# Optimization experiments

Measured on AMD Instinct MI355X. Metric: run time of the kernel, lower is better.

The kernel has to match this reference:

```python
import jax, jax.numpy as jnp
import numpy as np

N = 100000
E = 1600000
IN_FEATS = 512
H1, F1 = 8, 8          # layer1: 8 heads x 8 units
H2, F2 = 1, 40         # layer2: 1 head x out_feats
NEG_SLOPE = 0.2


def setup_inputs() -> dict:
    key = jax.random.key(0)
    ks = jax.random.split(key, 12)
    x = jax.random.normal(ks[0], (N, IN_FEATS), dtype=jnp.float32)
    src = jax.random.randint(ks[1], (E,), 0, N, dtype=jnp.int32)
    dst = jax.random.randint(ks[2], (E,), 0, N, dtype=jnp.int32)
    # Xavier-ish init for params
    W1 = jax.random.normal(ks[3], (IN_FEATS, H1 * F1), dtype=jnp.float32) * (1.0 / np.sqrt(IN_FEATS))
    al1 = jax.random.normal(ks[4], (H1, F1), dtype=jnp.float32) * 0.1
    ar1 = jax.random.normal(ks[5], (H1, F1), dtype=jnp.float32) * 0.1
    b1 = jnp.zeros((H1 * F1,), dtype=jnp.float32)
    W2 = jax.random.normal(ks[6], (H1 * F1, H2 * F2), dtype=jnp.float32) * (1.0 / np.sqrt(H1 * F1))
    al2 = jax.random.normal(ks[7], (H2, F2), dtype=jnp.float32) * 0.1
    ar2 = jax.random.normal(ks[8], (H2, F2), dtype=jnp.float32) * 0.1
    b2 = jnp.zeros((H2 * F2,), dtype=jnp.float32)
    return {"x": x, "src": src, "dst": dst,
            "W1": W1, "al1": al1, "ar1": ar1, "b1": b1,
            "W2": W2, "al2": al2, "ar2": ar2, "b2": b2}


def _gat_conv(feat, src, dst, W, al, ar, b, activation):
    """DGL-style GATConv (dropout disabled / eval mode)."""
    n = feat.shape[0]
    heads, fdim = al.shape
    h = (feat @ W).reshape(n, heads, fdim)            # [N, H, F]
    el = jnp.einsum('nhf,hf->nh', h, al)              # [N, H]
    er = jnp.einsum('nhf,hf->nh', h, ar)              # [N, H]
    e = jax.nn.leaky_relu(el[src] + er[dst], NEG_SLOPE)   # [E, H]
    # edge softmax over incoming edges of each dst node (numerically stable)
    m = jax.ops.segment_max(e, dst, num_segments=n)   # [N, H]
    ex = jnp.exp(e - m[dst])
    s = jax.ops.segment_sum(ex, dst, num_segments=n)  # [N, H]
    alpha = ex / s[dst]                               # [E, H]
    msg = h[src] * alpha[:, :, None]                  # [E, H, F]
    rst = jax.ops.segment_sum(msg, dst, num_segments=n)  # [N, H, F]
    rst = rst + b.reshape(1, heads, fdim)
    if activation is not None:
        rst = activation(rst)
    return rst


def reference(x, src, dst, W1, al1, ar1, b1, W2, al2, ar2, b2):
    h1 = _gat_conv(x, src, dst, W1, al1, ar1, b1, jax.nn.elu)   # [N, H1, F1]
    h1 = h1.reshape(x.shape[0], H1 * F1)                        # flatten(1)
    h2 = _gat_conv(h1, src, dst, W2, al2, ar2, b2, None)        # [N, 1, F2]
    logits = h2.mean(axis=1)                                    # [N, F2]
    return jax.nn.log_softmax(logits, axis=1)
```

## Files before the change

### kernel.cpp

```cpp
#include <hip/hip_runtime.h>
#include <cstdint>
#include <cstddef>

#define IN_F 512
#define C1 64
#define NH 8
#define FD 8
#define C2 40
#define NEG 0.2f

typedef __attribute__((ext_vector_type(8))) short bf16x8;
typedef __attribute__((ext_vector_type(4))) float f32x4;

__device__ inline unsigned short f32_to_bf16_rne(float f) {
    unsigned int u = __float_as_uint(f);
    unsigned int r = (u + 0x7FFFu + ((u >> 16) & 1u)) >> 16;
    return (unsigned short)r;
}
__device__ inline float bf16_to_f32(unsigned short s) {
    return __uint_as_float(((unsigned int)s) << 16);
}

__global__ __launch_bounds__(256) void hist_k(const int* __restrict__ dst, int* __restrict__ deg,
                                              int* __restrict__ pos, int E) {
    int e = blockIdx.x * 256 + threadIdx.x;
    if (e < E) pos[e] = atomicAdd(&deg[dst[e]], 1);
}

__global__ __launch_bounds__(1024) void scan_local_k(const int* __restrict__ deg, int* __restrict__ rowp,
                                                     int* __restrict__ bsums, int n) {
    __shared__ int tmp[1024];
    int tx = threadIdx.x;
    int i = blockIdx.x * 1024 + tx;
    int v = (i < n) ? deg[i] : 0;
    tmp[tx] = v;
    __syncthreads();
    for (int d = 1; d < 1024; d <<= 1) {
        int t = (tx >= d) ? tmp[tx - d] : 0;
        __syncthreads();
        tmp[tx] += t;
        __syncthreads();
    }
    if (i < n) rowp[i] = tmp[tx] - v;
    if (tx == 1023) bsums[blockIdx.x] = tmp[tx];
}

__global__ __launch_bounds__(128) void scan_sums_k(int* bsums, int nb) {
    __shared__ int tmp[128];
    int tx = threadIdx.x;
    int v = (tx < nb) ? bsums[tx] : 0;
    tmp[tx] = v;
    __syncthreads();
    for (int d = 1; d < 128; d <<= 1) {
        int t = (tx >= d) ? tmp[tx - d] : 0;
        __syncthreads();
        tmp[tx] += t;
        __syncthreads();
    }
    if (tx < nb) bsums[tx] = tmp[tx] - v;
}

__global__ __launch_bounds__(1024) void scan_add_k(int* rowp, const int* __restrict__ bsums, int n) {
    int i = blockIdx.x * 1024 + threadIdx.x;
    if (i < n) rowp[i] += bsums[blockIdx.x];
}

__global__ __launch_bounds__(256) void scatter_k(const int* __restrict__ src, const int* __restrict__ dst,
                                                 const int* __restrict__ rowp, const int* __restrict__ pos,
                                                 int* __restrict__ csr_src, int E) {
    int e = blockIdx.x * 256 + threadIdx.x;
    if (e >= E) return;
    csr_src[rowp[dst[e]] + pos[e]] = src[e];
}

__global__ __launch_bounds__(256) void wt_pre_k(const float* __restrict__ W1,
                                                unsigned short* __restrict__ wt_hi,
                                                unsigned short* __restrict__ wt_lo) {
    int id = blockIdx.x * 256 + threadIdx.x;
    if (id >= IN_F * C1) return;
    int col = id & (C1 - 1);
    int k = id >> 6;
    float w = W1[id];
    unsigned short hb = f32_to_bf16_rne(w);
    unsigned short lb = f32_to_bf16_rne(w - bf16_to_f32(hb));
    wt_hi[(size_t)col * IN_F + k] = hb;
    wt_lo[(size_t)col * IN_F + k] = lb;
}

__global__ __launch_bounds__(256) void gemm1_mfma_k(const float* __restrict__ x,
                                                    const unsigned short* __restrict__ wt_hi,
                                                    const unsigned short* __restrict__ wt_lo,
                                                    float* __restrict__ h, int N) {
    __shared__ alignas(16) unsigned short wlds[2][8192];
    const int tid = threadIdx.x;
    const int wave = tid >> 6, lane = tid & 63;
    const int m = lane & 15, q = lane >> 4;
    const int row = blockIdx.x * 64 + wave * 16 + m;
    const int row_c = row < N ? row : N - 1;
    const float* xp = x + (size_t)row_c * IN_F + q * 8;

    f32x4 acc[4];
#pragma unroll
    for (int ct = 0; ct < 4; ct++) acc[ct] = (f32x4){0.f, 0.f, 0.f, 0.f};
    float4 xr[2][4];

#define WLOAD(c, buf)                                                                              \
    {                                                                                              \
        _Pragma("unroll") for (int j_ = 0; j_ < 4; j_++) {                                         \
            int slot_ = j_ * 256 + wave * 64 + lane;                                               \
            const unsigned short* gbase_ = (slot_ < 512) ? wt_hi : wt_lo;                          \
            int s_ = slot_ & 511;                                                                  \
            int col_ = s_ & 63, kq_ = s_ >> 6;                                                     \
            const unsigned short* g_ = gbase_ + (size_t)col_ * IN_F + (c) * 64 + kq_ * 8;          \
            unsigned short* l_ = &wlds[buf][0] + (size_t)(j_ * 256 + wave * 64) * 8;               \
            __builtin_amdgcn_global_load_lds((const __attribute__((address_space(1))) unsigned int*)g_, \
                                             (__attribute__((address_space(3))) unsigned int*)l_,  \
                                             16, 0, 0);                                            \
        }                                                                                          \
    }
#define XLOAD(c, r)                                  \
    {                                                \
        const float* xsrc_ = xp + (c) * 64;          \
        (r)[0] = *(const float4*)(xsrc_);            \
        (r)[1] = *(const float4*)(xsrc_ + 4);        \
        (r)[2] = *(const float4*)(xsrc_ + 32);       \
        (r)[3] = *(const float4*)(xsrc_ + 36);       \
    }

    WLOAD(0, 0);
    XLOAD(0, xr[0]);

    for (int c = 0; c < 8; c++) {
        int p = c & 1;
        __syncthreads();
        if (c < 7) {
            WLOAD(c + 1, p ^ 1);
            XLOAD(c + 1, xr[p ^ 1]);
        }
#pragma unroll
        for (int ki = 0; ki < 2; ki++) {
            float f[8];
            f[0] = xr[p][ki * 2].x; f[1] = xr[p][ki * 2].y; f[2] = xr[p][ki * 2].z; f[3] = xr[p][ki * 2].w;
            f[4] = xr[p][ki * 2 + 1].x; f[5] = xr[p][ki * 2 + 1].y; f[6] = xr[p][ki * 2 + 1].z; f[7] = xr[p][ki * 2 + 1].w;
            unsigned int u[8], lu[8];
#pragma unroll
            for (int j = 0; j < 8; j++) u[j] = __float_as_uint(f[j]);
            union { uint4 u4; bf16x8 v; } H, L;
            H.u4.x = __builtin_amdgcn_perm(u[1], u[0], 0x07060302u);
            H.u4.y = __builtin_amdgcn_perm(u[3], u[2], 0x07060302u);
            H.u4.z = __builtin_amdgcn_perm(u[5], u[4], 0x07060302u);
            H.u4.w = __builtin_amdgcn_perm(u[7], u[6], 0x07060302u);
#pragma unroll
            for (int j = 0; j < 8; j++)
                lu[j] = __float_as_uint(f[j] - __uint_as_float(u[j] & 0xFFFF0000u));
            L.u4.x = __builtin_amdgcn_perm(lu[1], lu[0], 0x07060302u);
            L.u4.y = __builtin_amdgcn_perm(lu[3], lu[2], 0x07060302u);
            L.u4.z = __builtin_amdgcn_perm(lu[5], lu[4], 0x07060302u);
            L.u4.w = __builtin_amdgcn_perm(lu[7], lu[6], 0x07060302u);
            int kq = ki * 4 + q;
#pragma unroll
            for (int ct = 0; ct < 4; ct++) {
                int slot = kq * 64 + ct * 16 + m;
                bf16x8 bh = *(const bf16x8*)&wlds[p][slot * 8];
                bf16x8 bl = *(const bf16x8*)&wlds[p][4096 + slot * 8];
                acc[ct] = __builtin_amdgcn_mfma_f32_16x16x32_bf16(H.v, bh, acc[ct], 0, 0, 0);
                acc[ct] = __builtin_amdgcn_mfma_f32_16x16x32_bf16(L.v, bh, acc[ct], 0, 0, 0);
                acc[ct] = __builtin_amdgcn_mfma_f32_16x16x32_bf16(H.v, bl, acc[ct], 0, 0, 0);
            }
        }
    }
    int rbase = blockIdx.x * 64 + wave * 16 + q * 4;
#pragma unroll
    for (int r = 0; r < 4; r++) {
        int ro = rbase + r;
        if (ro < N) {
#pragma unroll
            for (int ct = 0; ct < 4; ct++)
                h[(size_t)ro * C1 + ct * 16 + m] = acc[ct][r];
        }
    }
#undef WLOAD
#undef XLOAD
}

__global__ __launch_bounds__(256) void attn1_k(const float* __restrict__ h, const float* __restrict__ al,
                                               const float* __restrict__ ar, float* __restrict__ el,
                                               float* __restrict__ er, int N) {
    int idx = blockIdx.x * 256 + threadIdx.x;
    if (idx >= N * NH) return;
    int n = idx >> 3, hd = idx & 7;
    const float4* hp = (const float4*)(h + (size_t)n * C1 + hd * FD);
    const float4* alp = (const float4*)(al + hd * FD);
    const float4* arp = (const float4*)(ar + hd * FD);
    float4 v0 = hp[0], v1 = hp[1];
    float4 a0 = alp[0], a1 = alp[1];
    float4 r0 = arp[0], r1 = arp[1];
    float e_l = v0.x * a0.x + v0.y * a0.y + v0.z * a0.z + v0.w * a0.w +
                v1.x * a1.x + v1.y * a1.y + v1.z * a1.z + v1.w * a1.w;
    float e_r = v0.x * r0.x + v0.y * r0.y + v0.z * r0.z + v0.w * r0.w +
                v1.x * r1.x + v1.y * r1.y + v1.z * r1.z + v1.w * r1.w;
    el[idx] = e_l;
    er[idx] = e_r;
}

__global__ __launch_bounds__(256) void l1_wave_k(const float* __restrict__ h,
                                                 const float* __restrict__ el, const float* __restrict__ er,
                                                 const int* __restrict__ rowp, const int* __restrict__ deg,
                                                 const int* __restrict__ csr_src, const float* __restrict__ b1,
                                                 float* __restrict__ h1out, int N) {
    int n = (blockIdx.x * 256 + threadIdx.x) >> 6;
    if (n >= N) return;
    int lane = threadIdx.x & 63;
    int hg = lane >> 3;
    int start = rowp[n], cnt = deg[n];
    float erd = er[n * NH + hg];
    float acc = 0.f, s = 0.f;
    int i = 0;
    for (; i + 4 <= cnt; i += 4) {
        const int* cp = csr_src + start + i;
        int sn0 = cp[0], sn1 = cp[1], sn2 = cp[2], sn3 = cp[3];
        float e0 = el[sn0 * NH + hg];
        float e1 = el[sn1 * NH + hg];
        float e2 = el[sn2 * NH + hg];
        float e3 = el[sn3 * NH + hg];
        float v0 = h[(size_t)sn0 * C1 + lane];
        float v1 = h[(size_t)sn1 * C1 + lane];
        float v2 = h[(size_t)sn2 * C1 + lane];
        float v3 = h[(size_t)sn3 * C1 + lane];
        e0 += erd; e1 += erd; e2 += erd; e3 += erd;
        e0 = e0 > 0.f ? e0 : NEG * e0;
        e1 = e1 > 0.f ? e1 : NEG * e1;
        e2 = e2 > 0.f ? e2 : NEG * e2;
        e3 = e3 > 0.f ? e3 : NEG * e3;
        float w0 = __expf(e0), w1 = __expf(e1), w2 = __expf(e2), w3 = __expf(e3);
        s += (w0 + w1) + (w2 + w3);
        acc += w0 * v0 + w1 * v1 + w2 * v2 + w3 * v3;
    }
    for (; i < cnt; i++) {
        int sn = csr_src[start + i];
        float e = el[sn * NH + hg] + erd;
        e = e > 0.f ? e : NEG * e;
        float w0 = __expf(e);
        s += w0;
        acc += w0 * h[(size_t)sn * C1 + lane];
    }
    float sinv = (s > 0.f) ? 1.f / s : 0.f;
    float o = acc * sinv + b1[lane];
    o = o > 0.f ? o : (__expf(o) - 1.f);
    h1out[(size_t)n * C1 + lane] = o;
}

__global__ __launch_bounds__(256) void gemm2_attn2_k(const float* __restrict__ h1, const float* __restrict__ W2,
                                                     const float* __restrict__ al2, const float* __restrict__ ar2,
                                                     float* __restrict__ h2pre, float* __restrict__ el2,
                                                     float* __restrict__ er2, int N) {
    __shared__ float ws[C1 * C2];
    __shared__ float hs[64][C1];
    __shared__ float h2s[64][C2];
    __shared__ float a2s[2 * C2];
    int t = threadIdx.x;
    int n0 = blockIdx.x * 64;
    for (int i = t; i < C1 * C2; i += 256) ws[i] = W2[i];
    if (t < C2) a2s[t] = al2[t];
    else if (t < 2 * C2) a2s[t] = ar2[t - C2];
    for (int i = t; i < 64 * 16; i += 256) {
        int r = i >> 4, c4 = i & 15;
        int n = n0 + r;
        float4 v = (n < N) ? *(const float4*)(h1 + (size_t)n * C1 + c4 * 4) : make_float4(0.f, 0.f, 0.f, 0.f);
        *(float4*)&hs[r][c4 * 4] = v;
    }
    __syncthreads();
    for (int o = t; o < 64 * C2; o += 256) {
        int r = o / C2, c = o % C2;
        float sum = 0.f;
#pragma unroll
        for (int k = 0; k < C1; k++) sum += hs[r][k] * ws[k * C2 + c];
        h2s[r][c] = sum;
        int nn = n0 + r;
        if (nn < N) h2pre[(size_t)nn * C2 + c] = sum;
    }
    __syncthreads();
    if (t < 64) {
        int nn = n0 + t;
        if (nn < N) {
            float e_l = 0.f, e_r = 0.f;
#pragma unroll
            for (int c = 0; c < C2; c++) {
                float v = h2s[t][c];
                e_l += v * a2s[c];
                e_r += v * a2s[C2 + c];
            }
            el2[nn] = e_l;
            er2[nn] = e_r;
        }
    }
}

__global__ __launch_bounds__(256) void l2_fused_k(const float* __restrict__ h2, const float* __restrict__ el,
                                                  const float* __restrict__ er, const int* __restrict__ rowp,
                                                  const int* __restrict__ deg, const int* __restrict__ csr_src,
                                                  const float* __restrict__ b2, float* __restrict__ out, int N) {
    int tid = threadIdx.x;
    int n = blockIdx.x * 32 + (tid >> 3);
    int sub = tid & 7;
    if (n >= N) return;
    int start = rowp[n], cnt = deg[n];
    float erd = er[n];
    float s = 0.f;
    float4 a4 = make_float4(0.f, 0.f, 0.f, 0.f);
    float a1 = 0.f;
    int i = 0;
    for (; i + 4 <= cnt; i += 4) {
        const int* cp = csr_src + start + i;
        int sn0 = cp[0], sn1 = cp[1], sn2 = cp[2], sn3 = cp[3];
        float e0 = el[sn0], e1 = el[sn1], e2 = el[sn2], e3 = el[sn3];
        const float* hp0 = h2 + (size_t)sn0 * C2;
        const float* hp1 = h2 + (size_t)sn1 * C2;
        const float* hp2 = h2 + (size_t)sn2 * C2;
        const float* hp3 = h2 + (size_t)sn3 * C2;
        float4 v0 = *(const float4*)(hp0 + sub * 4);
        float4 v1 = *(const float4*)(hp1 + sub * 4);
        float4 v2 = *(const float4*)(hp2 + sub * 4);
        float4 v3 = *(const float4*)(hp3 + sub * 4);
        float s0 = hp0[32 + sub], s1 = hp1[32 + sub], s2 = hp2[32 + sub], s3 = hp3[32 + sub];
        e0 += erd; e1 += erd; e2 += erd; e3 += erd;
        e0 = e0 > 0.f ? e0 : NEG * e0;
        e1 = e1 > 0.f ? e1 : NEG * e1;
        e2 = e2 > 0.f ? e2 : NEG * e2;
        e3 = e3 > 0.f ? e3 : NEG * e3;
        float w0 = __expf(e0), w1 = __expf(e1), w2 = __expf(e2), w3 = __expf(e3);
        s += (w0 + w1) + (w2 + w3);
        a4.x += w0 * v0.x + w1 * v1.x + w2 * v2.x + w3 * v3.x;
        a4.y += w0 * v0.y + w1 * v1.y + w2 * v2.y + w3 * v3.y;
        a4.z += w0 * v0.z + w1 * v1.z + w2 * v2.z + w3 * v3.z;
        a4.w += w0 * v0.w + w1 * v1.w + w2 * v2.w + w3 * v3.w;
        a1 += w0 * s0 + w1 * s1 + w2 * s2 + w3 * s3;
    }
    for (; i < cnt; i++) {
        int sn = csr_src[start + i];
        float e = el[sn] + erd;
        e = e > 0.f ? e : NEG * e;
        float w0 = __expf(e);
        s += w0;
        const float* hp = h2 + (size_t)sn * C2;
        float4 v = *(const float4*)(hp + sub * 4);
        a4.x += w0 * v.x; a4.y += w0 * v.y; a4.z += w0 * v.z; a4.w += w0 * v.w;
        a1 += w0 * hp[32 + sub];
    }
    float sinv = (s > 0.f) ? 1.f / s : 0.f;
    float4 bb = *(const float4*)(b2 + sub * 4);
    a4.x = a4.x * sinv + bb.x; a4.y = a4.y * sinv + bb.y;
    a4.z = a4.z * sinv + bb.z; a4.w = a4.w * sinv + bb.w;
    a1 = a1 * sinv + b2[32 + sub];
    float mx = fmaxf(fmaxf(fmaxf(a4.x, a4.y), fmaxf(a4.z, a4.w)), a1);
#pragma unroll
    for (int off = 1; off < 8; off <<= 1) mx = fmaxf(mx, __shfl_xor(mx, off, 8));
    float se = __expf(a4.x - mx) + __expf(a4.y - mx) + __expf(a4.z - mx) + __expf(a4.w - mx) + __expf(a1 - mx);
#pragma unroll
    for (int off = 1; off < 8; off <<= 1) se += __shfl_xor(se, off, 8);
    float ls = __logf(se) + mx;
    float* op = out + (size_t)n * C2;
    *(float4*)(op + sub * 4) = make_float4(a4.x - ls, a4.y - ls, a4.z - ls, a4.w - ls);
    op[32 + sub] = a1 - ls;
}

extern "C" void kernel_launch(void* const* d_in, const int* in_sizes, int n_in,
                              void* d_out, int out_size, void* d_ws, size_t ws_size,
                              hipStream_t stream) {
    (void)n_in; (void)out_size; (void)ws_size;
    const float* x   = (const float*)d_in[0];
    const int*   src = (const int*)d_in[1];
    const int*   dst = (const int*)d_in[2];
    const float* W1  = (const float*)d_in[3];
    const float* al1 = (const float*)d_in[4];
    const float* ar1 = (const float*)d_in[5];
    const float* b1  = (const float*)d_in[6];
    const float* W2  = (const float*)d_in[7];
    const float* al2 = (const float*)d_in[8];
    const float* ar2 = (const float*)d_in[9];
    const float* b2  = (const float*)d_in[10];
    float* out = (float*)d_out;
    const int N = in_sizes[0] / IN_F;
    const int E = in_sizes[1];

    char* w = (char*)d_ws;
    auto alloc = [&](size_t bytes) -> char* {
        char* p = w;
        w += (bytes + 255) & ~(size_t)255;
        return p;
    };
    int* deg     = (int*)alloc((size_t)N * 4);
    int* rowp    = (int*)alloc((size_t)N * 4);
    int* bsums   = (int*)alloc(512);
    int* pos     = (int*)alloc((size_t)E * 4);
    int* csr_src = (int*)alloc((size_t)E * 4);
    unsigned short* wt_hi = (unsigned short*)alloc((size_t)IN_F * C1 * 2);
    unsigned short* wt_lo = (unsigned short*)alloc((size_t)IN_F * C1 * 2);
    float* h1pre = (float*)alloc((size_t)N * C1 * 4);
    float* el1   = (float*)alloc((size_t)N * NH * 4);
    float* er1   = (float*)alloc((size_t)N * NH * 4);
    float* h1    = (float*)alloc((size_t)N * C1 * 4);
    float* h2pre = (float*)alloc((size_t)N * C2 * 4);
    float* el2   = (float*)alloc((size_t)N * 4);
    float* er2   = (float*)alloc((size_t)N * 4);

    hipMemsetAsync(deg, 0, (size_t)N * 4, stream);

    int ebl = (E + 255) / 256;
    int nb = (N + 1023) / 1024;
    hist_k<<<ebl, 256, 0, stream>>>(dst, deg, pos, E);
    scan_local_k<<<nb, 1024, 0, stream>>>(deg, rowp, bsums, N);
    scan_sums_k<<<1, 128, 0, stream>>>(bsums, nb);
    scan_add_k<<<nb, 1024, 0, stream>>>(rowp, bsums, N);
    scatter_k<<<ebl, 256, 0, stream>>>(src, dst, rowp, pos, csr_src, E);

    wt_pre_k<<<(IN_F * C1 + 255) / 256, 256, 0, stream>>>(W1, wt_hi, wt_lo);
    gemm1_mfma_k<<<(N + 63) / 64, 256, 0, stream>>>(x, wt_hi, wt_lo, h1pre, N);
    attn1_k<<<(N * NH + 255) / 256, 256, 0, stream>>>(h1pre, al1, ar1, el1, er1, N);
    l1_wave_k<<<(N * 64 + 255) / 256, 256, 0, stream>>>(h1pre, el1, er1, rowp, deg, csr_src, b1, h1, N);
    gemm2_attn2_k<<<(N + 63) / 64, 256, 0, stream>>>(h1, W2, al2, ar2, h2pre, el2, er2, N);
    l2_fused_k<<<(N + 31) / 32, 256, 0, stream>>>(h2pre, el2, er2, rowp, deg, csr_src, b2, out, N);
}
```

Baseline: 635.6 us.

## Store layer features as bf16 to halve gather bandwidth in both aggregations

Layer-1 projected features and layer-2 projected features are now written as bf16 instead of fp32. Layer-2 rows are padded to 64 entries so each 8-lane group loads one aligned 16-byte vector. The edge-aggregation kernels gather these bf16 rows and convert to fp32 before accumulating, which halves the bytes fetched per random neighbour access. The cost is reduced precision in the attention logits and messages, and layer 1 now does 2-byte scalar loads per lane.

```diff
diff --git a/kernel.cpp b/kernel.cpp
--- a/kernel.cpp
+++ b/kernel.cpp
@@ -90,7 +90,7 @@
 __global__ __launch_bounds__(256) void gemm1_mfma_k(const float* __restrict__ x,
                                                     const unsigned short* __restrict__ wt_hi,
                                                     const unsigned short* __restrict__ wt_lo,
-                                                    float* __restrict__ h, int N) {
+                                                    unsigned short* __restrict__ hb_out, int N) {
     __shared__ alignas(16) unsigned short wlds[2][8192];
     const int tid = threadIdx.x;
     const int wave = tid >> 6, lane = tid & 63;
@@ -176,34 +176,36 @@
         if (ro < N) {
 #pragma unroll
             for (int ct = 0; ct < 4; ct++)
-                h[(size_t)ro * C1 + ct * 16 + m] = acc[ct][r];
+                hb_out[(size_t)ro * C1 + ct * 16 + m] = f32_to_bf16_rne(acc[ct][r]);
         }
     }
 #undef WLOAD
 #undef XLOAD
 }
 
-__global__ __launch_bounds__(256) void attn1_k(const float* __restrict__ h, const float* __restrict__ al,
-                                               const float* __restrict__ ar, float* __restrict__ el,
-                                               float* __restrict__ er, int N) {
+__global__ __launch_bounds__(256) void attn1_k(const unsigned short* __restrict__ hb,
+                                               const float* __restrict__ al, const float* __restrict__ ar,
+                                               float* __restrict__ el, float* __restrict__ er, int N) {
     int idx = blockIdx.x * 256 + threadIdx.x;
     if (idx >= N * NH) return;
     int n = idx >> 3, hd = idx & 7;
-    const float4* hp = (const float4*)(h + (size_t)n * C1 + hd * FD);
+    bf16x8 v = *(const bf16x8*)(hb + (size_t)n * C1 + hd * FD);
     const float4* alp = (const float4*)(al + hd * FD);
     const float4* arp = (const float4*)(ar + hd * FD);
-    float4 v0 = hp[0], v1 = hp[1];
     float4 a0 = alp[0], a1 = alp[1];
     float4 r0 = arp[0], r1 = arp[1];
-    float e_l = v0.x * a0.x + v0.y * a0.y + v0.z * a0.z + v0.w * a0.w +
-                v1.x * a1.x + v1.y * a1.y + v1.z * a1.z + v1.w * a1.w;
-    float e_r = v0.x * r0.x + v0.y * r0.y + v0.z * r0.z + v0.w * r0.w +
-                v1.x * r1.x + v1.y * r1.y + v1.z * r1.z + v1.w * r1.w;
+    float f[8];
+#pragma unroll
+    for (int j = 0; j < 8; j++) f[j] = bf16_to_f32((unsigned short)v[j]);
+    float e_l = f[0] * a0.x + f[1] * a0.y + f[2] * a0.z + f[3] * a0.w +
+                f[4] * a1.x + f[5] * a1.y + f[6] * a1.z + f[7] * a1.w;
+    float e_r = f[0] * r0.x + f[1] * r0.y + f[2] * r0.z + f[3] * r0.w +
+                f[4] * r1.x + f[5] * r1.y + f[6] * r1.z + f[7] * r1.w;
     el[idx] = e_l;
     er[idx] = e_r;
 }
 
-__global__ __launch_bounds__(256) void l1_wave_k(const float* __restrict__ h,
+__global__ __launch_bounds__(256) void l1_wave_k(const unsigned short* __restrict__ hb,
                                                  const float* __restrict__ el, const float* __restrict__ er,
                                                  const int* __restrict__ rowp, const int* __restrict__ deg,
                                                  const int* __restrict__ csr_src, const float* __restrict__ b1,
@@ -223,10 +225,10 @@
         float e1 = el[sn1 * NH + hg];
         float e2 = el[sn2 * NH + hg];
         float e3 = el[sn3 * NH + hg];
-        float v0 = h[(size_t)sn0 * C1 + lane];
-        float v1 = h[(size_t)sn1 * C1 + lane];
-        float v2 = h[(size_t)sn2 * C1 + lane];
-        float v3 = h[(size_t)sn3 * C1 + lane];
+        unsigned short q0 = hb[(size_t)sn0 * C1 + lane];
+        unsigned short q1 = hb[(size_t)sn1 * C1 + lane];
+        unsigned short q2 = hb[(size_t)sn2 * C1 + lane];
+        unsigned short q3 = hb[(size_t)sn3 * C1 + lane];
         e0 += erd; e1 += erd; e2 += erd; e3 += erd;
         e0 = e0 > 0.f ? e0 : NEG * e0;
         e1 = e1 > 0.f ? e1 : NEG * e1;
@@ -234,7 +236,7 @@
         e3 = e3 > 0.f ? e3 : NEG * e3;
         float w0 = __expf(e0), w1 = __expf(e1), w2 = __expf(e2), w3 = __expf(e3);
         s += (w0 + w1) + (w2 + w3);
-        acc += w0 * v0 + w1 * v1 + w2 * v2 + w3 * v3;
+        acc += w0 * bf16_to_f32(q0) + w1 * bf16_to_f32(q1) + w2 * bf16_to_f32(q2) + w3 * bf16_to_f32(q3);
     }
     for (; i < cnt; i++) {
         int sn = csr_src[start + i];
@@ -242,7 +244,7 @@
         e = e > 0.f ? e : NEG * e;
         float w0 = __expf(e);
         s += w0;
-        acc += w0 * h[(size_t)sn * C1 + lane];
+        acc += w0 * bf16_to_f32(hb[(size_t)sn * C1 + lane]);
     }
     float sinv = (s > 0.f) ? 1.f / s : 0.f;
     float o = acc * sinv + b1[lane];
@@ -252,7 +254,7 @@
 
 __global__ __launch_bounds__(256) void gemm2_attn2_k(const float* __restrict__ h1, const float* __restrict__ W2,
                                                      const float* __restrict__ al2, const float* __restrict__ ar2,
-                                                     float* __restrict__ h2pre, float* __restrict__ el2,
+                                                     unsigned short* __restrict__ h2b, float* __restrict__ el2,
                                                      float* __restrict__ er2, int N) {
     __shared__ float ws[C1 * C2];
     __shared__ float hs[64][C1];
@@ -276,10 +278,13 @@
 #pragma unroll
         for (int k = 0; k < C1; k++) sum += hs[r][k] * ws[k * C2 + c];
         h2s[r][c] = sum;
+    }
+    __syncthreads();
+    for (int o = t; o < 64 * 64; o += 256) {
+        int r = o >> 6, c = o & 63;
         int nn = n0 + r;
-        if (nn < N) h2pre[(size_t)nn * C2 + c] = sum;
-    }
-    __syncthreads();
+        if (nn < N) h2b[(size_t)nn * 64 + c] = (c < C2) ? f32_to_bf16_rne(h2s[r][c]) : (unsigned short)0;
+    }
     if (t < 64) {
         int nn = n0 + t;
         if (nn < N) {
@@ -296,10 +301,11 @@
     }
 }
 
-__global__ __launch_bounds__(256) void l2_fused_k(const float* __restrict__ h2, const float* __restrict__ el,
-                                                  const float* __restrict__ er, const int* __restrict__ rowp,
-                                                  const int* __restrict__ deg, const int* __restrict__ csr_src,
-                                                  const float* __restrict__ b2, float* __restrict__ out, int N) {
+__global__ __launch_bounds__(256) void l2_fused_k(const unsigned short* __restrict__ h2b,
+                                                  const float* __restrict__ el, const float* __restrict__ er,
+                                                  const int* __restrict__ rowp, const int* __restrict__ deg,
+                                                  const int* __restrict__ csr_src, const float* __restrict__ b2,
+                                                  float* __restrict__ out, int N) {
     int tid = threadIdx.x;
     int n = blockIdx.x * 32 + (tid >> 3);
     int sub = tid & 7;
@@ -307,22 +313,18 @@
     int start = rowp[n], cnt = deg[n];
     float erd = er[n];
     float s = 0.f;
-    float4 a4 = make_float4(0.f, 0.f, 0.f, 0.f);
-    float a1 = 0.f;
+    float acc[8];
+#pragma unroll
+    for (int j = 0; j < 8; j++) acc[j] = 0.f;
     int i = 0;
     for (; i + 4 <= cnt; i += 4) {
         const int* cp = csr_src + start + i;
         int sn0 = cp[0], sn1 = cp[1], sn2 = cp[2], sn3 = cp[3];
         float e0 = el[sn0], e1 = el[sn1], e2 = el[sn2], e3 = el[sn3];
-        const float* hp0 = h2 + (size_t)sn0 * C2;
-        const float* hp1 = h2 + (size_t)sn1 * C2;
-        const float* hp2 = h2 + (size_t)sn2 * C2;
-        const float* hp3 = h2 + (size_t)sn3 * C2;
-        float4 v0 = *(const float4*)(hp0 + sub * 4);
-        float4 v1 = *(const float4*)(hp1 + sub * 4);
-        float4 v2 = *(const float4*)(hp2 + sub * 4);
-        float4 v3 = *(const float4*)(hp3 + sub * 4);
-        float s0 = hp0[32 + sub], s1 = hp1[32 + sub], s2 = hp2[32 + sub], s3 = hp3[32 + sub];
+        bf16x8 v0 = *(const bf16x8*)(h2b + (size_t)sn0 * 64 + sub * 8);
+        bf16x8 v1 = *(const bf16x8*)(h2b + (size_t)sn1 * 64 + sub * 8);
+        bf16x8 v2 = *(const bf16x8*)(h2b + (size_t)sn2 * 64 + sub * 8);
+        bf16x8 v3 = *(const bf16x8*)(h2b + (size_t)sn3 * 64 + sub * 8);
         e0 += erd; e1 += erd; e2 += erd; e3 += erd;
         e0 = e0 > 0.f ? e0 : NEG * e0;
         e1 = e1 > 0.f ? e1 : NEG * e1;
@@ -330,11 +332,11 @@
         e3 = e3 > 0.f ? e3 : NEG * e3;
         float w0 = __expf(e0), w1 = __expf(e1), w2 = __expf(e2), w3 = __expf(e3);
         s += (w0 + w1) + (w2 + w3);
-        a4.x += w0 * v0.x + w1 * v1.x + w2 * v2.x + w3 * v3.x;
-        a4.y += w0 * v0.y + w1 * v1.y + w2 * v2.y + w3 * v3.y;
-        a4.z += w0 * v0.z + w1 * v1.z + w2 * v2.z + w3 * v3.z;
-        a4.w += w0 * v0.w + w1 * v1.w + w2 * v2.w + w3 * v3.w;
-        a1 += w0 * s0 + w1 * s1 + w2 * s2 + w3 * s3;
+#pragma unroll
+        for (int j = 0; j < 8; j++) {
+            acc[j] += w0 * bf16_to_f32((unsigned short)v0[j]) + w1 * bf16_to_f32((unsigned short)v1[j]) +
+                      w2 * bf16_to_f32((unsigned short)v2[j]) + w3 * bf16_to_f32((unsigned short)v3[j]);
+        }
     }
     for (; i < cnt; i++) {
         int sn = csr_src[start + i];
@@ -342,26 +344,33 @@
         e = e > 0.f ? e : NEG * e;
         float w0 = __expf(e);
         s += w0;
-        const float* hp = h2 + (size_t)sn * C2;
-        float4 v = *(const float4*)(hp + sub * 4);
-        a4.x += w0 * v.x; a4.y += w0 * v.y; a4.z += w0 * v.z; a4.w += w0 * v.w;
-        a1 += w0 * hp[32 + sub];
+        bf16x8 v = *(const bf16x8*)(h2b + (size_t)sn * 64 + sub * 8);
+#pragma unroll
+        for (int j = 0; j < 8; j++) acc[j] += w0 * bf16_to_f32((unsigned short)v[j]);
     }
     float sinv = (s > 0.f) ? 1.f / s : 0.f;
-    float4 bb = *(const float4*)(b2 + sub * 4);
-    a4.x = a4.x * sinv + bb.x; a4.y = a4.y * sinv + bb.y;
-    a4.z = a4.z * sinv + bb.z; a4.w = a4.w * sinv + bb.w;
-    a1 = a1 * sinv + b2[32 + sub];
-    float mx = fmaxf(fmaxf(fmaxf(a4.x, a4.y), fmaxf(a4.z, a4.w)), a1);
+    float vals[8];
+#pragma unroll
+    for (int j = 0; j < 8; j++) {
+        int c = sub * 8 + j;
+        vals[j] = (c < C2) ? (acc[j] * sinv + b2[c]) : -1e30f;
+    }
+    float mx = vals[0];
+#pragma unroll
+    for (int j = 1; j < 8; j++) mx = fmaxf(mx, vals[j]);
 #pragma unroll
     for (int off = 1; off < 8; off <<= 1) mx = fmaxf(mx, __shfl_xor(mx, off, 8));
-    float se = __expf(a4.x - mx) + __expf(a4.y - mx) + __expf(a4.z - mx) + __expf(a4.w - mx) + __expf(a1 - mx);
+    float se = 0.f;
+#pragma unroll
+    for (int j = 0; j < 8; j++) se += __expf(vals[j] - mx);
 #pragma unroll
     for (int off = 1; off < 8; off <<= 1) se += __shfl_xor(se, off, 8);
     float ls = __logf(se) + mx;
-    float* op = out + (size_t)n * C2;
-    *(float4*)(op + sub * 4) = make_float4(a4.x - ls, a4.y - ls, a4.z - ls, a4.w - ls);
-    op[32 + sub] = a1 - ls;
+    if (sub < 5) {
+        float* op = out + (size_t)n * C2 + sub * 8;
+        *(float4*)(op) = make_float4(vals[0] - ls, vals[1] - ls, vals[2] - ls, vals[3] - ls);
+        *(float4*)(op + 4) = make_float4(vals[4] - ls, vals[5] - ls, vals[6] - ls, vals[7] - ls);
+    }
 }
 
 extern "C" void kernel_launch(void* const* d_in, const int* in_sizes, int n_in,
@@ -396,11 +405,11 @@
     int* csr_src = (int*)alloc((size_t)E * 4);
     unsigned short* wt_hi = (unsigned short*)alloc((size_t)IN_F * C1 * 2);
     unsigned short* wt_lo = (unsigned short*)alloc((size_t)IN_F * C1 * 2);
-    float* h1pre = (float*)alloc((size_t)N * C1 * 4);
+    unsigned short* hb    = (unsigned short*)alloc((size_t)N * C1 * 2);
     float* el1   = (float*)alloc((size_t)N * NH * 4);
     float* er1   = (float*)alloc((size_t)N * NH * 4);
     float* h1    = (float*)alloc((size_t)N * C1 * 4);
-    float* h2pre = (float*)alloc((size_t)N * C2 * 4);
+    unsigned short* h2b = (unsigned short*)alloc((size_t)N * 64 * 2);
     float* el2   = (float*)alloc((size_t)N * 4);
     float* er2   = (float*)alloc((size_t)N * 4);
 
@@ -415,9 +424,9 @@
     scatter_k<<<ebl, 256, 0, stream>>>(src, dst, rowp, pos, csr_src, E);
 
     wt_pre_k<<<(IN_F * C1 + 255) / 256, 256, 0, stream>>>(W1, wt_hi, wt_lo);
-    gemm1_mfma_k<<<(N + 63) / 64, 256, 0, stream>>>(x, wt_hi, wt_lo, h1pre, N);
-    attn1_k<<<(N * NH + 255) / 256, 256, 0, stream>>>(h1pre, al1, ar1, el1, er1, N);
-    l1_wave_k<<<(N * 64 + 255) / 256, 256, 0, stream>>>(h1pre, el1, er1, rowp, deg, csr_src, b1, h1, N);
-    gemm2_attn2_k<<<(N + 63) / 64, 256, 0, stream>>>(h1, W2, al2, ar2, h2pre, el2, er2, N);
-    l2_fused_k<<<(N + 31) / 32, 256, 0, stream>>>(h2pre, el2, er2, rowp, deg, csr_src, b2, out, N);
-}
+    gemm1_mfma_k<<<(N + 63) / 64, 256, 0, stream>>>(x, wt_hi, wt_lo, hb, N);
+    attn1_k<<<(N * NH + 255) / 256, 256, 0, stream>>>(hb, al1, ar1, el1, er1, N);
+    l1_wave_k<<<(N * 64 + 255) / 256, 256, 0, stream>>>(hb, el1, er1, rowp, deg, csr_src, b1, h1, N);
+    gemm2_attn2_k<<<(N + 63) / 64, 256, 0, stream>>>(h1, W2, al2, ar2, h2b, el2, er2, N);
+    l2_fused_k<<<(N + 31) / 32, 256, 0, stream>>>(h2b, el2, er2, rowp, deg, csr_src, b2, out, N);
+}
```

Result: faster. 612.7 us (-3.6%).
